# Kernel optimization log

Measured on AMD Instinct MI355X. Metric: run time of the kernel, lower is better.

The kernel has to match this reference:

```python
import jax, jax.numpy as jnp
import numpy as np

T, B, D, O, U = 64, 32768, 6, 3, 6


def setup_inputs() -> dict:
    key = jax.random.key(0)
    ks = jax.random.split(key, 8)
    measurements = jax.random.normal(ks[0], (T, B, O), dtype=jnp.float32)
    inputs_seq = jax.random.normal(ks[1], (T, B, U), dtype=jnp.float32)
    mean0 = jax.random.normal(ks[2], (B, D), dtype=jnp.float32)
    # initial covariance: 0.1 * I, positive definite
    cov0 = jnp.broadcast_to(0.1 * jnp.eye(D, dtype=jnp.float32), (B, D, D))
    # linear motion model params (jacobian = A), kept near-stable
    A = jnp.eye(D, dtype=jnp.float32) + 0.01 * jax.random.normal(ks[3], (D, D), dtype=jnp.float32)
    Bm = 0.1 * jax.random.normal(ks[4], (D, U), dtype=jnp.float32)
    Q_tril = jnp.tril(0.05 * jax.random.normal(ks[5], (D, D), dtype=jnp.float32)) + 0.1 * jnp.eye(D, dtype=jnp.float32)
    # linear measurement model params (jacobian = C)
    C = jax.random.normal(ks[6], (O, D), dtype=jnp.float32) / np.sqrt(D)
    R_tril = jnp.tril(0.05 * jax.random.normal(ks[7], (O, O), dtype=jnp.float32)) + 0.1 * jnp.eye(O, dtype=jnp.float32)
    return {"measurements": measurements, "inputs_seq": inputs_seq, "mean0": mean0,
            "cov0": cov0, "A": A, "Bm": Bm, "Q_tril": Q_tril, "C": C, "R_tril": R_tril}


def reference(measurements, inputs_seq, mean0, cov0, A, Bm, Q_tril, C, R_tril):
    Qc = Q_tril @ Q_tril.T            # (D, D) dynamics covariance
    Rc = R_tril @ R_tril.T            # (O, O) measurement covariance
    I = jnp.eye(mean0.shape[-1], dtype=mean0.dtype)

    def step(carry, xs):
        mean, cov = carry             # (B, D), (B, D, D)
        z, u = xs                     # (B, O), (B, U)
        # --- predict ---
        pred_mean = mean @ A.T + u @ Bm.T                        # (B, D)
        pred_cov = jnp.einsum('ij,bjk,lk->bil', A, cov, A) + Qc  # (B, D, D)
        # --- update ---
        pred_meas = pred_mean @ C.T                              # (B, O)
        innovation = z - pred_meas
        S = jnp.einsum('ij,bjk,lk->bil', C, pred_cov, C) + Rc    # (B, O, O)
        PCt = jnp.einsum('bij,kj->bik', pred_cov, C)             # (B, D, O)
        K = PCt @ jnp.linalg.inv(S)                              # (B, D, O)
        new_mean = pred_mean + jnp.einsum('bij,bj->bi', K, innovation)
        new_cov = (I - jnp.einsum('bij,jk->bik', K, C)) @ pred_cov
        return (new_mean, new_cov), new_mean

    (_, _), means = jax.lax.scan(step, (mean0, cov0), (measurements, inputs_seq))
    return means  # (T, B, D)
```

## Files before the change

### kernel.cpp

```cpp
#include <hip/hip_runtime.h>


#define T_STEPS 64
#define BATCH   32768
#define NCOEF   90
#define NCHUNK  8
#define CLEN    8

#define G_OFF   23040
#define WS_NEED (G_OFF + 1152)

__device__ __forceinline__ float rdlane(float v, int lane) {
    return __int_as_float(__builtin_amdgcn_readlane(__float_as_int(v), lane));
}

__global__ __launch_bounds__(64) void ekf_precompute(
    const float* __restrict__ cov0, const float* __restrict__ Ag,
    const float* __restrict__ Bg,   const float* __restrict__ Qtg,
    const float* __restrict__ Cg,   const float* __restrict__ Rtg,
    float* __restrict__ coef, float* __restrict__ Gmat, int writeG)
{
    __shared__ float sA[36], sB[36], sC[18], sQt[36], sRt[9];
    __shared__ float Qc[36], Rc[9];
    __shared__ float Mall[T_STEPS * 36];
    const int tid = threadIdx.x;

    if (tid < 36) { sA[tid] = Ag[tid]; sB[tid] = Bg[tid]; sQt[tid] = Qtg[tid]; }
    if (tid < 18) sC[tid] = Cg[tid];
    if (tid < 9)  sRt[tid] = Rtg[tid];
    __syncthreads();

    if (tid < 36) {
        int i = tid / 6, j = tid % 6; float s = 0.f;
        #pragma unroll
        for (int k = 0; k < 6; ++k) s += sQt[i*6+k] * sQt[j*6+k];
        Qc[tid] = s;
    } else if (tid < 45) {
        int q = tid - 36, i = q / 3, j = q % 3; float s = 0.f;
        #pragma unroll
        for (int k = 0; k < 3; ++k) s += sRt[i*3+k] * sRt[j*3+k];
        Rc[q] = s;
    }
    __syncthreads();

    const int i6 = tid / 6, j6 = tid % 6;
    const int i3 = tid / 3, j3 = tid % 3;
    const int qS = (tid >= 36 && tid < 45) ? tid - 36 : 0;
    const int sa = qS / 3, sb = qS % 3;

    float Ai[6], Aj[6], Acol[6], Bcol[6], Cst[18], Crow[6], Ca[6];
    float qcv = 0.f, rcv = 0.f;
    #pragma unroll
    for (int l = 0; l < 6; ++l) { Ai[l]=0.f; Aj[l]=0.f; Acol[l]=0.f; Bcol[l]=0.f; Crow[l]=0.f; Ca[l]=0.f; }
    #pragma unroll
    for (int l = 0; l < 18; ++l) Cst[l] = 0.f;

    if (tid < 36) {
        #pragma unroll
        for (int l = 0; l < 6; ++l) {
            Ai[l] = sA[i6*6+l]; Aj[l] = sA[j6*6+l];
            Acol[l] = sA[l*6+j6]; Bcol[l] = sB[l*6+j6];
        }
        #pragma unroll
        for (int l = 0; l < 18; ++l) Cst[l] = sC[l];
        qcv = Qc[tid];
    }
    if (tid < 18) {
        #pragma unroll
        for (int l = 0; l < 6; ++l) Crow[l] = sC[j3*6+l];
    }
    if (tid >= 36 && tid < 45) {
        #pragma unroll
        for (int l = 0; l < 6; ++l) Ca[l] = sC[sa*6+l];
        rcv = Rc[qS];
    }

    float Preg = 0.f;
    if (tid < 36) Preg = cov0[tid];
    __syncthreads();

    for (int t = 0; t < T_STEPS; ++t) {
        float Pf[36];
        #pragma unroll
        for (int e = 0; e < 36; ++e) Pf[e] = rdlane(Preg, e);
        float p1 = qcv;
        #pragma unroll
        for (int k = 0; k < 6; ++k) {
            float tmp = 0.f;
            #pragma unroll
            for (int l = 0; l < 6; ++l) tmp += Pf[k*6+l] * Aj[l];
            p1 += Ai[k] * tmp;
        }

        float p1r[6], p1col[6];
        #pragma unroll
        for (int l = 0; l < 6; ++l) p1r[l]   = __shfl(p1, i3*6 + l);
        #pragma unroll
        for (int k = 0; k < 6; ++k) p1col[k] = __shfl(p1, k*6 + j6);

        float pct = p1r[0]*Crow[0] + p1r[1]*Crow[1] + p1r[2]*Crow[2]
                  + p1r[3]*Crow[3] + p1r[4]*Crow[4] + p1r[5]*Crow[5];

        float pcol[6], Pi0, Pi1, Pi2;
        #pragma unroll
        for (int l = 0; l < 6; ++l) pcol[l] = __shfl(pct, l*3 + sb);
        Pi0 = __shfl(pct, i6*3 + 0);
        Pi1 = __shfl(pct, i6*3 + 1);
        Pi2 = __shfl(pct, i6*3 + 2);

        float sv = rcv;
        #pragma unroll
        for (int l = 0; l < 6; ++l) sv += Ca[l] * pcol[l];

        float a  = rdlane(sv, 36), b  = rdlane(sv, 37), c  = rdlane(sv, 38);
        float d  = rdlane(sv, 39), e  = rdlane(sv, 40), f  = rdlane(sv, 41);
        float g  = rdlane(sv, 42), h  = rdlane(sv, 43), i9 = rdlane(sv, 44);
        float idet = 1.0f / (a*(e*i9-f*h) - b*(d*i9-f*g) + c*(d*h-e*g));
        float s0 =  (e*i9-f*h)*idet, s1 = -(b*i9-c*h)*idet, s2 =  (b*f-c*e)*idet;
        float s3 = -(d*i9-f*g)*idet, s4 =  (a*i9-c*g)*idet, s5 = -(a*f-c*d)*idet;
        float s6 =  (d*h-e*g)*idet,  s7 = -(a*h-b*g)*idet,  s8 =  (a*e-b*d)*idet;

        float K0 = Pi0*s0 + Pi1*s3 + Pi2*s6;
        float K1 = Pi0*s1 + Pi1*s4 + Pi2*s7;
        float K2 = Pi0*s2 + Pi1*s5 + Pi2*s8;

        float ik[6];
        #pragma unroll
        for (int k = 0; k < 6; ++k)
            ik[k] = ((i6 == k) ? 1.f : 0.f)
                  - (K0*Cst[0*6+k] + K1*Cst[1*6+k] + K2*Cst[2*6+k]);

        float mo = 0.f, no = 0.f, pn = 0.f;
        #pragma unroll
        for (int k = 0; k < 6; ++k) {
            mo += ik[k] * Acol[k];
            no += ik[k] * Bcol[k];
            pn += ik[k] * p1col[k];
        }

        if (tid < 36) {
            coef[t*NCOEF + tid]      = mo;
            coef[t*NCOEF + 36 + tid] = no;
            if (j6 < 3)
                coef[t*NCOEF + 72 + i6*3 + j6] = (j6 == 0 ? K0 : (j6 == 1 ? K1 : K2));
            Mall[t*36 + tid] = mo;
        }
        Preg = pn;
    }
    __syncthreads();

    if (writeG) {
        const int im = (tid < 36) ? i6 : 0;
        for (int cch = 0; cch < NCHUNK; ++cch) {
            float Gv = (tid < 36) ? Mall[(cch*CLEN)*36 + tid] : 0.f;
            for (int s = 1; s < CLEN; ++s) {
                float gk[6];
                #pragma unroll
                for (int k = 0; k < 6; ++k) gk[k] = __shfl(Gv, k*6 + j6);
                float acc = 0.f;
                #pragma unroll
                for (int k = 0; k < 6; ++k)
                    acc += Mall[(cch*CLEN + s)*36 + im*6 + k] * gk[k];
                Gv = acc;
            }
            if (tid < 36) Gmat[cch*36 + tid] = Gv;
        }
    }
}

__global__ __launch_bounds__(512) void ekf_scan(
    const float* __restrict__ z, const float* __restrict__ u,
    const float* __restrict__ mean0, const float* __restrict__ coef,
    const float* __restrict__ Gmat, float* __restrict__ out)
{
    __shared__ float gl[NCHUNK][64][6];
    const int lane = threadIdx.x & 63;
    const int c    = __builtin_amdgcn_readfirstlane(threadIdx.x >> 6);
    const int b    = blockIdx.x * 64 + lane;

    float zz[CLEN][3], uu[CLEN][6];
    float m[6] = {0.f, 0.f, 0.f, 0.f, 0.f, 0.f};

    #pragma unroll
    for (int s = 0; s < CLEN; ++s) {
        const int t = c * CLEN + s;
        const float* cf = coef + t * NCOEF;
        const int base  = t * BATCH + b;

        const float*  zp = z + (size_t)base * 3;
        const float2* up = (const float2*)(u + (size_t)base * 6);
        zz[s][0] = zp[0]; zz[s][1] = zp[1]; zz[s][2] = zp[2];
        float2 u01 = up[0], u23 = up[1], u45 = up[2];
        uu[s][0]=u01.x; uu[s][1]=u01.y; uu[s][2]=u23.x;
        uu[s][3]=u23.y; uu[s][4]=u45.x; uu[s][5]=u45.y;

        float nm[6];
        #pragma unroll
        for (int i = 0; i < 6; ++i) {
            float s2 = 0.f;
            #pragma unroll
            for (int j = 0; j < 6; ++j) s2 += cf[i*6+j] * m[j];
            #pragma unroll
            for (int j = 0; j < 6; ++j) s2 += cf[36 + i*6 + j] * uu[s][j];
            #pragma unroll
            for (int j = 0; j < 3; ++j) s2 += cf[72 + i*3 + j] * zz[s][j];
            nm[i] = s2;
        }
        #pragma unroll
        for (int i = 0; i < 6; ++i) m[i] = nm[i];
    }

    #pragma unroll
    for (int i = 0; i < 6; ++i) gl[c][lane][i] = m[i];
    __syncthreads();

    float bm[6];
    {
        const float2* mp = (const float2*)(mean0 + (size_t)b * 6);
        float2 a0 = mp[0], a1 = mp[1], a2 = mp[2];
        bm[0]=a0.x; bm[1]=a0.y; bm[2]=a1.x; bm[3]=a1.y; bm[4]=a2.x; bm[5]=a2.y;
    }
    for (int cc = 0; cc < c; ++cc) {
        const float* G = Gmat + cc * 36;
        float gv[6];
        #pragma unroll
        for (int i = 0; i < 6; ++i) gv[i] = gl[cc][lane][i];
        float nm[6];
        #pragma unroll
        for (int i = 0; i < 6; ++i) {
            float s2 = gv[i];
            #pragma unroll
            for (int j = 0; j < 6; ++j) s2 += G[i*6+j] * bm[j];
            nm[i] = s2;
        }
        #pragma unroll
        for (int i = 0; i < 6; ++i) bm[i] = nm[i];
    }

    #pragma unroll
    for (int s = 0; s < CLEN; ++s) {
        const int t = c * CLEN + s;
        const float* cf = coef + t * NCOEF;
        const int base  = t * BATCH + b;

        float nm[6];
        #pragma unroll
        for (int i = 0; i < 6; ++i) {
            float s2 = 0.f;
            #pragma unroll
            for (int j = 0; j < 6; ++j) s2 += cf[i*6+j] * bm[j];
            #pragma unroll
            for (int j = 0; j < 6; ++j) s2 += cf[36 + i*6 + j] * uu[s][j];
            #pragma unroll
            for (int j = 0; j < 3; ++j) s2 += cf[72 + i*3 + j] * zz[s][j];
            nm[i] = s2;
        }

        float2* op = (float2*)(out + (size_t)base * 6);
        op[0] = make_float2(nm[0], nm[1]);
        op[1] = make_float2(nm[2], nm[3]);
        op[2] = make_float2(nm[4], nm[5]);

        #pragma unroll
        for (int i = 0; i < 6; ++i) bm[i] = nm[i];
    }
}

__global__ __launch_bounds__(128) void ekf_mean(
    const float* __restrict__ z, const float* __restrict__ u,
    const float* __restrict__ mean0, const float* __restrict__ coef,
    float* __restrict__ out)
{
    __shared__ float sc[T_STEPS * NCOEF];
    const int tid = threadIdx.x;
    for (int idx = tid; idx < T_STEPS * NCOEF; idx += 128) sc[idx] = coef[idx];

    const int b = blockIdx.x * 128 + tid;
    float m[6];
    {
        const float2* mp = (const float2*)(mean0 + b * 6);
        float2 a0 = mp[0], a1 = mp[1], a2 = mp[2];
        m[0]=a0.x; m[1]=a0.y; m[2]=a1.x; m[3]=a1.y; m[4]=a2.x; m[5]=a2.y;
    }
    __syncthreads();

    #pragma unroll 2
    for (int t = 0; t < T_STEPS; ++t) {
        const float* cf  = &sc[t * NCOEF];
        const int base   = t * BATCH + b;
        const float*  zp = z + base * 3;
        const float2* up = (const float2*)(u + (size_t)base * 6);

        float zzv[3] = { zp[0], zp[1], zp[2] };
        float2 u01 = up[0], u23 = up[1], u45 = up[2];
        float uuv[6] = { u01.x, u01.y, u23.x, u23.y, u45.x, u45.y };

        float nm[6];
        #pragma unroll
        for (int i = 0; i < 6; ++i) {
            float s = 0.f;
            #pragma unroll
            for (int j = 0; j < 6; ++j) s += cf[i*6+j] * m[j];
            #pragma unroll
            for (int j = 0; j < 6; ++j) s += cf[36 + i*6 + j] * uuv[j];
            #pragma unroll
            for (int j = 0; j < 3; ++j) s += cf[72 + i*3 + j] * zzv[j];
            nm[i] = s;
        }

        float2* op = (float2*)(out + (size_t)base * 6);
        op[0] = make_float2(nm[0], nm[1]);
        op[1] = make_float2(nm[2], nm[3]);
        op[2] = make_float2(nm[4], nm[5]);

        #pragma unroll
        for (int i = 0; i < 6; ++i) m[i] = nm[i];
    }
}

extern "C" void kernel_launch(void* const* d_in, const int* in_sizes, int n_in,
                              void* d_out, int out_size, void* d_ws, size_t ws_size,
                              hipStream_t stream) {
    const float* meas  = (const float*)d_in[0];
    const float* useq  = (const float*)d_in[1];
    const float* mean0 = (const float*)d_in[2];
    const float* cov0  = (const float*)d_in[3];
    const float* A     = (const float*)d_in[4];
    const float* Bm    = (const float*)d_in[5];
    const float* Qt    = (const float*)d_in[6];
    const float* C     = (const float*)d_in[7];
    const float* Rt    = (const float*)d_in[8];
    float* out  = (float*)d_out;

    float* coef = (float*)d_ws;
    float* Gmat = (float*)((char*)d_ws + G_OFF);

    const bool scan_path = (ws_size >= (size_t)WS_NEED);

    ekf_precompute<<<1, 64, 0, stream>>>(cov0, A, Bm, Qt, C, Rt, coef, Gmat,
                                         scan_path ? 1 : 0);
    if (scan_path) {
        ekf_scan<<<BATCH / 64, 512, 0, stream>>>(meas, useq, mean0, coef, Gmat, out);
    } else {
        ekf_mean<<<BATCH / 128, 128, 0, stream>>>(meas, useq, mean0, coef, out);
    }
}
```

Before: 198.5 us.

## Split chunked scan into two global-memory passes with finer chunks

Replaces the single fused scan kernel, which shared chunk partial states through LDS, with two kernels. The first computes per-chunk zero-start states and writes them to workspace; the second combines preceding chunk states via the G matrices and emits outputs. It uses 16 chunks of 4 steps when workspace allows, giving more parallelism and fewer registers per thread. It also rewrites the covariance predict in precompute to use shuffles instead of 36 readlanes. The cost is extra global traffic for the chunk states, z and u being read twice, and a second launch.

Measured after the change: 191.0 us. 3.8% less time.

```diff
diff --git a/kernel.cpp b/kernel.cpp
--- a/kernel.cpp
+++ b/kernel.cpp
@@ -4,11 +4,11 @@
 #define T_STEPS 64
 #define BATCH   32768
 #define NCOEF   90
-#define NCHUNK  8
-#define CLEN    8
 
 #define G_OFF   23040
-#define WS_NEED (G_OFF + 1152)
+#define GV_OFF  (G_OFF + 16*36*4)
+#define WS_N16  (GV_OFF + 16 * BATCH * 6 * 4)
+#define WS_N8   (GV_OFF +  8 * BATCH * 6 * 4)
 
 __device__ __forceinline__ float rdlane(float v, int lane) {
     return __int_as_float(__builtin_amdgcn_readlane(__float_as_int(v), lane));
@@ -18,7 +18,7 @@
     const float* __restrict__ cov0, const float* __restrict__ Ag,
     const float* __restrict__ Bg,   const float* __restrict__ Qtg,
     const float* __restrict__ Cg,   const float* __restrict__ Rtg,
-    float* __restrict__ coef, float* __restrict__ Gmat, int writeG)
+    float* __restrict__ coef, float* __restrict__ Gmat, int writeG, int clen)
 {
     __shared__ float sA[36], sB[36], sC[18], sQt[36], sRt[9];
     __shared__ float Qc[36], Rc[9];
@@ -80,17 +80,17 @@
     __syncthreads();
 
     for (int t = 0; t < T_STEPS; ++t) {
-        float Pf[36];
-        #pragma unroll
-        for (int e = 0; e < 36; ++e) Pf[e] = rdlane(Preg, e);
+        float prow[6];
+        #pragma unroll
+        for (int l = 0; l < 6; ++l) prow[l] = __shfl(Preg, i6*6 + l);
+        float Tv = prow[0]*Aj[0] + prow[1]*Aj[1] + prow[2]*Aj[2]
+                 + prow[3]*Aj[3] + prow[4]*Aj[4] + prow[5]*Aj[5];
+        float tcol[6];
+        #pragma unroll
+        for (int k = 0; k < 6; ++k) tcol[k] = __shfl(Tv, k*6 + j6);
         float p1 = qcv;
         #pragma unroll
-        for (int k = 0; k < 6; ++k) {
-            float tmp = 0.f;
-            #pragma unroll
-            for (int l = 0; l < 6; ++l) tmp += Pf[k*6+l] * Aj[l];
-            p1 += Ai[k] * tmp;
-        }
+        for (int k = 0; k < 6; ++k) p1 += Ai[k] * tcol[k];
 
         float p1r[6], p1col[6];
         #pragma unroll
@@ -151,16 +151,17 @@
 
     if (writeG) {
         const int im = (tid < 36) ? i6 : 0;
-        for (int cch = 0; cch < NCHUNK; ++cch) {
-            float Gv = (tid < 36) ? Mall[(cch*CLEN)*36 + tid] : 0.f;
-            for (int s = 1; s < CLEN; ++s) {
+        const int nch = T_STEPS / clen;
+        for (int cch = 0; cch < nch; ++cch) {
+            float Gv = (tid < 36) ? Mall[(cch*clen)*36 + tid] : 0.f;
+            for (int s = 1; s < clen; ++s) {
                 float gk[6];
                 #pragma unroll
                 for (int k = 0; k < 6; ++k) gk[k] = __shfl(Gv, k*6 + j6);
                 float acc = 0.f;
                 #pragma unroll
                 for (int k = 0; k < 6; ++k)
-                    acc += Mall[(cch*CLEN + s)*36 + im*6 + k] * gk[k];
+                    acc += Mall[(cch*clen + s)*36 + im*6 + k] * gk[k];
                 Gv = acc;
             }
             if (tid < 36) Gmat[cch*36 + tid] = Gv;
@@ -168,32 +169,30 @@
     }
 }
 
-__global__ __launch_bounds__(512) void ekf_scan(
+template<int LCLEN>
+__global__ __launch_bounds__(256) void ekf_gpass(
     const float* __restrict__ z, const float* __restrict__ u,
-    const float* __restrict__ mean0, const float* __restrict__ coef,
-    const float* __restrict__ Gmat, float* __restrict__ out)
+    const float* __restrict__ coef, float* __restrict__ g)
 {
-    __shared__ float gl[NCHUNK][64][6];
-    const int lane = threadIdx.x & 63;
-    const int c    = __builtin_amdgcn_readfirstlane(threadIdx.x >> 6);
-    const int b    = blockIdx.x * 64 + lane;
-
-    float zz[CLEN][3], uu[CLEN][6];
-    float m[6] = {0.f, 0.f, 0.f, 0.f, 0.f, 0.f};
-
-    #pragma unroll
-    for (int s = 0; s < CLEN; ++s) {
-        const int t = c * CLEN + s;
-        const float* cf = coef + t * NCOEF;
-        const int base  = t * BATCH + b;
-
+    const int c = blockIdx.y;
+    const int b = blockIdx.x * 256 + threadIdx.x;
+
+    float zz[LCLEN][3], uu[LCLEN][6];
+    #pragma unroll
+    for (int s = 0; s < LCLEN; ++s) {
+        const int base = (c * LCLEN + s) * BATCH + b;
         const float*  zp = z + (size_t)base * 3;
         const float2* up = (const float2*)(u + (size_t)base * 6);
         zz[s][0] = zp[0]; zz[s][1] = zp[1]; zz[s][2] = zp[2];
         float2 u01 = up[0], u23 = up[1], u45 = up[2];
         uu[s][0]=u01.x; uu[s][1]=u01.y; uu[s][2]=u23.x;
         uu[s][3]=u23.y; uu[s][4]=u45.x; uu[s][5]=u45.y;
-
+    }
+
+    float m[6] = {0.f, 0.f, 0.f, 0.f, 0.f, 0.f};
+    #pragma unroll
+    for (int s = 0; s < LCLEN; ++s) {
+        const float* cf = coef + (c * LCLEN + s) * NCOEF;
         float nm[6];
         #pragma unroll
         for (int i = 0; i < 6; ++i) {
@@ -210,9 +209,33 @@
         for (int i = 0; i < 6; ++i) m[i] = nm[i];
     }
 
-    #pragma unroll
-    for (int i = 0; i < 6; ++i) gl[c][lane][i] = m[i];
-    __syncthreads();
+    float2* gp = (float2*)(g + ((size_t)c * BATCH + b) * 6);
+    gp[0] = make_float2(m[0], m[1]);
+    gp[1] = make_float2(m[2], m[3]);
+    gp[2] = make_float2(m[4], m[5]);
+}
+
+template<int LCLEN>
+__global__ __launch_bounds__(256) void ekf_opass(
+    const float* __restrict__ z, const float* __restrict__ u,
+    const float* __restrict__ mean0, const float* __restrict__ coef,
+    const float* __restrict__ Gmat, const float* __restrict__ g,
+    float* __restrict__ out)
+{
+    const int c = blockIdx.y;
+    const int b = blockIdx.x * 256 + threadIdx.x;
+
+    float zz[LCLEN][3], uu[LCLEN][6];
+    #pragma unroll
+    for (int s = 0; s < LCLEN; ++s) {
+        const int base = (c * LCLEN + s) * BATCH + b;
+        const float*  zp = z + (size_t)base * 3;
+        const float2* up = (const float2*)(u + (size_t)base * 6);
+        zz[s][0] = zp[0]; zz[s][1] = zp[1]; zz[s][2] = zp[2];
+        float2 u01 = up[0], u23 = up[1], u45 = up[2];
+        uu[s][0]=u01.x; uu[s][1]=u01.y; uu[s][2]=u23.x;
+        uu[s][3]=u23.y; uu[s][4]=u45.x; uu[s][5]=u45.y;
+    }
 
     float bm[6];
     {
@@ -220,11 +243,13 @@
         float2 a0 = mp[0], a1 = mp[1], a2 = mp[2];
         bm[0]=a0.x; bm[1]=a0.y; bm[2]=a1.x; bm[3]=a1.y; bm[4]=a2.x; bm[5]=a2.y;
     }
+
+    #pragma unroll 2
     for (int cc = 0; cc < c; ++cc) {
         const float* G = Gmat + cc * 36;
-        float gv[6];
-        #pragma unroll
-        for (int i = 0; i < 6; ++i) gv[i] = gl[cc][lane][i];
+        const float2* gp = (const float2*)(g + ((size_t)cc * BATCH + b) * 6);
+        float2 g01 = gp[0], g23 = gp[1], g45 = gp[2];
+        float gv[6] = { g01.x, g01.y, g23.x, g23.y, g45.x, g45.y };
         float nm[6];
         #pragma unroll
         for (int i = 0; i < 6; ++i) {
@@ -238,8 +263,8 @@
     }
 
     #pragma unroll
-    for (int s = 0; s < CLEN; ++s) {
-        const int t = c * CLEN + s;
+    for (int s = 0; s < LCLEN; ++s) {
+        const int t = c * LCLEN + s;
         const float* cf = coef + t * NCOEF;
         const int base  = t * BATCH + b;
 
@@ -334,13 +359,22 @@
 
     float* coef = (float*)d_ws;
     float* Gmat = (float*)((char*)d_ws + G_OFF);
-
-    const bool scan_path = (ws_size >= (size_t)WS_NEED);
+    float* gvec = (float*)((char*)d_ws + GV_OFF);
+
+    int clen = 0;
+    if (ws_size >= (size_t)WS_N16)      clen = 4;
+    else if (ws_size >= (size_t)WS_N8)  clen = 8;
 
     ekf_precompute<<<1, 64, 0, stream>>>(cov0, A, Bm, Qt, C, Rt, coef, Gmat,
-                                         scan_path ? 1 : 0);
-    if (scan_path) {
-        ekf_scan<<<BATCH / 64, 512, 0, stream>>>(meas, useq, mean0, coef, Gmat, out);
+                                         clen ? 1 : 0, clen ? clen : 8);
+    if (clen == 4) {
+        dim3 grid(BATCH / 256, T_STEPS / 4);
+        ekf_gpass<4><<<grid, 256, 0, stream>>>(meas, useq, coef, gvec);
+        ekf_opass<4><<<grid, 256, 0, stream>>>(meas, useq, mean0, coef, Gmat, gvec, out);
+    } else if (clen == 8) {
+        dim3 grid(BATCH / 256, T_STEPS / 8);
+        ekf_gpass<8><<<grid, 256, 0, stream>>>(meas, useq, coef, gvec);
+        ekf_opass<8><<<grid, 256, 0, stream>>>(meas, useq, mean0, coef, Gmat, gvec, out);
     } else {
         ekf_mean<<<BATCH / 128, 128, 0, stream>>>(meas, useq, mean0, coef, out);
     }
```
